# Performance work log

Measured on AMD Instinct MI355X. Metric: run time of the kernel, lower is better.

The kernel has to match this reference:

```python
import jax, jax.numpy as jnp
import numpy as np

N_SLOTS = 256   # memory slots
M_UNITS = 32    # memory word size
CTRL = 256      # LSTM controller units
N_IN = 8        # input features
N_OUT = 8
N_SHIFTS = 1
SHIFT_W = 2 * N_SHIFTS + 1          # 3 shift weights
ADDR = M_UNITS + 2 + SHIFT_W + 1    # key + beta + gate + shift + gamma = 38
CLIP = 20.0
EPS = 1e-8


def _lstm(x, h, c, Wk, Wr, b):
    z = x @ Wk + h @ Wr + b
    i, f, g, o = jnp.split(z, 4, axis=-1)  # keras gate order: i, f, c, o
    c = jax.nn.sigmoid(f) * c + jax.nn.sigmoid(i) * jnp.tanh(g)
    h = jax.nn.sigmoid(o) * jnp.tanh(c)
    return h, c


def _address(ho, w_prev, M):
    # ho: [B, ADDR] raw head outputs; M: [B, N, Mu]; w_prev: [B, N]
    k = jnp.tanh(ho[:, :M_UNITS])
    beta = jax.nn.softplus(ho[:, M_UNITS:M_UNITS + 1])
    g = jax.nn.sigmoid(ho[:, M_UNITS + 1:M_UNITS + 2])
    s = jax.nn.softmax(ho[:, M_UNITS + 2:M_UNITS + 2 + SHIFT_W], axis=-1)
    gamma = 1.0 + jax.nn.softplus(ho[:, ADDR - 1:ADDR])
    # content addressing via cosine similarity
    sim = jnp.einsum('bnm,bm->bn', M, k)
    sim = sim / (jnp.linalg.norm(M, axis=-1) * jnp.linalg.norm(k, axis=-1, keepdims=True) + EPS)
    w_c = jax.nn.softmax(beta * sim, axis=-1)
    # interpolation gate
    w_g = g * w_c + (1.0 - g) * w_prev
    # circular shift convolution over offsets [-N_SHIFTS..N_SHIFTS]
    w_s = sum(s[:, j:j + 1] * jnp.roll(w_g, j - N_SHIFTS, axis=-1) for j in range(SHIFT_W))
    # sharpening
    w_p = w_s ** gamma
    return w_p / (jnp.sum(w_p, axis=-1, keepdims=True) + EPS)


def setup_inputs() -> dict:
    key = jax.random.key(0)
    ks = jax.random.split(key, 10)
    B, T = 512, 64
    in_dim = N_IN + M_UNITS  # 40
    def w(k, shape, fan_in):
        return jax.random.normal(k, shape, jnp.float32) / np.sqrt(fan_in)
    return {
        'X': jax.random.normal(ks[0], (B, T, N_IN), jnp.float32),
        'lstm_Wk': w(ks[1], (in_dim, 4 * CTRL), in_dim),
        'lstm_Wr': w(ks[2], (CTRL, 4 * CTRL), CTRL),
        'lstm_b': jnp.zeros((4 * CTRL,), jnp.float32),
        'read_W': w(ks[3], (CTRL, ADDR), CTRL),
        'read_b': jnp.zeros((ADDR,), jnp.float32),
        'write_W': w(ks[4], (CTRL, ADDR + 2 * M_UNITS), CTRL),
        'write_b': jnp.zeros((ADDR + 2 * M_UNITS,), jnp.float32),
        'out_W': w(ks[5], (M_UNITS + CTRL, N_OUT), M_UNITS + CTRL),
        'out_b': jnp.zeros((N_OUT,), jnp.float32),
        'read_init': jax.random.normal(ks[6], (1, M_UNITS), jnp.float32),
        'wr_init': jax.random.normal(ks[7], (1, N_SLOTS), jnp.float32),
        'ww_init': jax.random.normal(ks[8], (1, N_SLOTS), jnp.float32),
    }


def reference(X, lstm_Wk, lstm_Wr, lstm_b, read_W, read_b, write_W, write_b,
              out_W, out_b, read_init, wr_init, ww_init):
    B = X.shape[0]
    M0 = jnp.full((B, N_SLOTS, M_UNITS), 1e-6, X.dtype)
    R0 = jnp.broadcast_to(jnp.tanh(read_init), (B, M_UNITS))
    Wr0 = jnp.broadcast_to(jax.nn.softmax(wr_init, axis=-1), (B, N_SLOTS))
    Ww0 = jnp.broadcast_to(jax.nn.softmax(ww_init, axis=-1), (B, N_SLOTS))
    h0 = jnp.zeros((B, CTRL), X.dtype)
    c0 = jnp.zeros((B, CTRL), X.dtype)

    def step(carry, x):
        M, R, Wr, Ww, h, c = carry
        h, c = _lstm(jnp.concatenate([x, R], axis=1), h, c, lstm_Wk, lstm_Wr, lstm_b)
        Z = jnp.clip(h, -CLIP, CLIP)
        # read head (uses pre-write memory, as in cell.call)
        Wr = _address(Z @ read_W + read_b, Wr, M)
        R = jnp.einsum('bn,bnm->bm', Wr, M)
        # write head: erase then add
        wo = Z @ write_W + write_b
        Ww = _address(wo[:, :ADDR], Ww, M)
        E = jax.nn.sigmoid(wo[:, ADDR:ADDR + M_UNITS])
        A = jnp.tanh(wo[:, ADDR + M_UNITS:ADDR + 2 * M_UNITS])
        M = M * (1.0 - jnp.einsum('bn,bm->bnm', Ww, E)) + jnp.einsum('bn,bm->bnm', Ww, A)
        Y = jnp.clip(jnp.concatenate([R, Z], axis=1) @ out_W + out_b, -CLIP, CLIP)
        return (M, R, Wr, Ww, h, c), Y

    _, Ys = jax.lax.scan(step, (M0, R0, Wr0, Ww0, h0, c0), jnp.swapaxes(X, 0, 1))
    return jnp.swapaxes(Ys, 0, 1)  # [B, T, N_OUT]
```

## Files before the change

### kernel.cpp

```cpp
#include <hip/hip_runtime.h>
#include <math.h>


#define NSLOT  256
#define MU     32
#define MPAD   33
#define TSTEPS 64
#define EPSF   1e-8f

__device__ __forceinline__ float sigf(float x){ return 1.0f/(1.0f + expf(-x)); }
__device__ __forceinline__ float softplusf_(float x){ return fmaxf(x,0.0f) + log1pf(expf(-fabsf(x))); }

__device__ __forceinline__ float wred_sum(float v){
  #pragma unroll
  for (int m = 32; m >= 1; m >>= 1) v += __shfl_xor(v, m, 64);
  return v;
}
__device__ __forceinline__ float wred_max(float v){
  #pragma unroll
  for (int m = 32; m >= 1; m >>= 1) v = fmaxf(v, __shfl_xor(v, m, 64));
  return v;
}

__device__ __forceinline__ float grp_red_sum(float v, float* red, int wave, int lane, int g2){
  v = wred_sum(v);
  if (lane == 0) red[wave] = v;
  __syncthreads();
  return red[4*g2] + red[4*g2+1] + red[4*g2+2] + red[4*g2+3];
}
__device__ __forceinline__ float grp_red_max(float v, float* red, int wave, int lane, int g2){
  v = wred_max(v);
  if (lane == 0) red[wave] = v;
  __syncthreads();
  return fmaxf(fmaxf(red[4*g2], red[4*g2+1]), fmaxf(red[4*g2+2], red[4*g2+3]));
}

struct Smem {
  float M[2][NSLOT][MPAD];
  float zp[2][2][1024];
  float h[2][256];
  float c[2][256];
  float hob[2][140];
  float xcat[2][40];
  float wr[2][NSLOT];
  float ww[2][NSLOT];
  float wg[2][2][NSLOT];
  float k[2][2][MU];
  float E[2][MU];
  float A[2][MU];
  float R[2][MU];
  float hpart[2][2][140];
  float rpart[2][8][MU];
  float red[3][8];
};

__device__ void address_head(int g2, int n2, int wave, int lane, int head,
                             const float* ho, float* wst, const float* Mg,
                             Smem& s)
{
  float beta  = softplusf_(ho[32]);
  float gg    = sigf(ho[33]);
  float r0 = ho[34], r1 = ho[35], r2 = ho[36];
  float m3 = fmaxf(r0, fmaxf(r1, r2));
  float e0 = expf(r0-m3), e1 = expf(r1-m3), e2 = expf(r2-m3);
  float inv3 = 1.0f/(e0+e1+e2);
  float s0 = e0*inv3, s1 = e1*inv3, s2 = e2*inv3;
  float gamma = 1.0f + softplusf_(ho[37]);

  float* kbuf  = &s.k[head][g2][0];
  float* wgbuf = &s.wg[head][g2][0];

  if (n2 < MU) kbuf[n2] = tanhf(ho[n2]);
  __syncthreads();

  float kn = 0.0f;
  #pragma unroll
  for (int m = 0; m < MU; ++m){ float kv = kbuf[m]; kn = fmaf(kv, kv, kn); }
  kn = sqrtf(kn);

  const float* Mr = Mg + n2*MPAD;
  float dot = 0.0f, mm = 0.0f;
  #pragma unroll
  for (int m = 0; m < MU; ++m){ float mv = Mr[m]; dot = fmaf(mv, kbuf[m], dot); mm = fmaf(mv, mv, mm); }
  float sim = dot / (sqrtf(mm)*kn + EPSF);

  float bs = beta * sim;
  float mx = grp_red_max(bs, s.red[0], wave, lane, g2);
  float ex = expf(bs - mx);
  float sm = grp_red_sum(ex, s.red[1], wave, lane, g2);
  float wc = ex / sm;

  float wgv = fmaf(gg, wc, (1.0f - gg)*wst[n2]);
  wgbuf[n2] = wgv;
  __syncthreads();

  float ws = s0*wgbuf[(n2+1)&255] + s1*wgbuf[n2] + s2*wgbuf[(n2-1)&255];

  float wp = powf(ws, gamma);
  float sp = grp_red_sum(wp, s.red[2], wave, lane, g2);
  wst[n2] = wp / (sp + EPSF);
}

__global__ __launch_bounds__(512)
void ntm_fused(const float* __restrict__ X,
               const float* __restrict__ Wk,   const float* __restrict__ Wr,
               const float* __restrict__ Lb,
               const float* __restrict__ rW,   const float* __restrict__ rb,
               const float* __restrict__ wW,   const float* __restrict__ wb,
               const float* __restrict__ oW,   const float* __restrict__ ob,
               const float* __restrict__ rInit,
               const float* __restrict__ wrI,  const float* __restrict__ wwI,
               float* __restrict__ Y)
{
  __shared__ Smem s;

  const int tid  = threadIdx.x;
  const int g2   = tid >> 8;
  const int n2   = tid & 255;
  const int wave = tid >> 6;
  const int lane = tid & 63;
  const int hf   = g2;
  const int bB   = blockIdx.x * 2;

  {
    for (int m = 0; m < MU; ++m) s.M[g2][n2][m] = 1e-6f;
    s.h[g2][n2] = 0.0f;
    s.c[g2][n2] = 0.0f;
    if (n2 < MU) s.R[g2][n2] = tanhf(rInit[n2]);
    float mx = -1e30f;
    for (int i = 0; i < NSLOT; ++i) mx = fmaxf(mx, wrI[i]);
    float sm = 0.0f;
    for (int i = 0; i < NSLOT; ++i) sm += expf(wrI[i] - mx);
    s.wr[g2][n2] = expf(wrI[n2] - mx) / sm;
    mx = -1e30f;
    for (int i = 0; i < NSLOT; ++i) mx = fmaxf(mx, wwI[i]);
    sm = 0.0f;
    for (int i = 0; i < NSLOT; ++i) sm += expf(wwI[i] - mx);
    s.ww[g2][n2] = expf(wwI[n2] - mx) / sm;
  }
  __syncthreads();

  for (int t = 0; t < TSTEPS; ++t) {
    if (n2 < 40) {
      s.xcat[g2][n2] = (n2 < 8) ? X[((bB + g2)*TSTEPS + t)*8 + n2]
                                : s.R[g2][n2 - 8];
    }
    __syncthreads();

    {
      const int c0 = n2 * 4;
      float a0x=0.f,a0y=0.f,a0z=0.f,a0w=0.f;
      float a1x=0.f,a1y=0.f,a1z=0.f,a1w=0.f;
      if (hf == 0) {
        #pragma unroll 4
        for (int i = 0; i < 40; ++i) {
          float4 w = *(const float4*)&Wk[i*1024 + c0];
          float x0 = s.xcat[0][i], x1 = s.xcat[1][i];
          a0x=fmaf(w.x,x0,a0x); a0y=fmaf(w.y,x0,a0y); a0z=fmaf(w.z,x0,a0z); a0w=fmaf(w.w,x0,a0w);
          a1x=fmaf(w.x,x1,a1x); a1y=fmaf(w.y,x1,a1y); a1z=fmaf(w.z,x1,a1z); a1w=fmaf(w.w,x1,a1w);
        }
        #pragma unroll 4
        for (int i = 0; i < 108; ++i) {
          float4 w = *(const float4*)&Wr[i*1024 + c0];
          float h0 = s.h[0][i], h1 = s.h[1][i];
          a0x=fmaf(w.x,h0,a0x); a0y=fmaf(w.y,h0,a0y); a0z=fmaf(w.z,h0,a0z); a0w=fmaf(w.w,h0,a0w);
          a1x=fmaf(w.x,h1,a1x); a1y=fmaf(w.y,h1,a1y); a1z=fmaf(w.z,h1,a1z); a1w=fmaf(w.w,h1,a1w);
        }
        float4 b = *(const float4*)&Lb[c0];
        a0x+=b.x; a0y+=b.y; a0z+=b.z; a0w+=b.w;
        a1x+=b.x; a1y+=b.y; a1z+=b.z; a1w+=b.w;
      } else {
        #pragma unroll 4
        for (int i = 108; i < 256; ++i) {
          float4 w = *(const float4*)&Wr[i*1024 + c0];
          float h0 = s.h[0][i], h1 = s.h[1][i];
          a0x=fmaf(w.x,h0,a0x); a0y=fmaf(w.y,h0,a0y); a0z=fmaf(w.z,h0,a0z); a0w=fmaf(w.w,h0,a0w);
          a1x=fmaf(w.x,h1,a1x); a1y=fmaf(w.y,h1,a1y); a1z=fmaf(w.z,h1,a1z); a1w=fmaf(w.w,h1,a1w);
        }
      }
      float* z0 = &s.zp[hf][0][c0];
      float* z1 = &s.zp[hf][1][c0];
      z0[0]=a0x; z0[1]=a0y; z0[2]=a0z; z0[3]=a0w;
      z1[0]=a1x; z1[1]=a1y; z1[2]=a1z; z1[3]=a1w;
    }
    __syncthreads();

    {
      float zi = s.zp[0][g2][n2      ] + s.zp[1][g2][n2      ];
      float zf = s.zp[0][g2][n2 + 256] + s.zp[1][g2][n2 + 256];
      float zg = s.zp[0][g2][n2 + 512] + s.zp[1][g2][n2 + 512];
      float zo = s.zp[0][g2][n2 + 768] + s.zp[1][g2][n2 + 768];
      float cn = sigf(zf)*s.c[g2][n2] + sigf(zi)*tanhf(zg);
      float hn = sigf(zo)*tanhf(cn);
      s.c[g2][n2] = cn;
      s.h[g2][n2] = hn;
    }
    __syncthreads();

    if (n2 < 140) {
      const float* Wp; int stride, cc;
      if (n2 < 38) { Wp = rW; stride = 38;  cc = n2; }
      else         { Wp = wW; stride = 102; cc = n2 - 38; }
      const int i0 = hf * 128;
      float acc0 = 0.0f, acc1 = 0.0f;
      #pragma unroll 4
      for (int ii = 0; ii < 128; ++ii) {
        int i = i0 + ii;
        float wv = Wp[i*stride + cc];
        acc0 = fmaf(wv, s.h[0][i], acc0);
        acc1 = fmaf(wv, s.h[1][i], acc1);
      }
      s.hpart[hf][0][n2] = acc0;
      s.hpart[hf][1][n2] = acc1;
    }
    __syncthreads();
    if (n2 < 140) {
      float bias = (n2 < 38) ? rb[n2] : wb[n2 - 38];
      s.hob[g2][n2] = s.hpart[0][g2][n2] + s.hpart[1][g2][n2] + bias;
    }
    __syncthreads();

    if (n2 < MU) {
      s.E[g2][n2] = sigf(s.hob[g2][76 + n2]);
      s.A[g2][n2] = tanhf(s.hob[g2][108 + n2]);
    }

    address_head(g2, n2, wave, lane, 0, &s.hob[g2][0],  &s.wr[g2][0],
                 &s.M[g2][0][0], s);
    address_head(g2, n2, wave, lane, 1, &s.hob[g2][38], &s.ww[g2][0],
                 &s.M[g2][0][0], s);

    {
      const int chunk = n2 >> 5;
      const int m     = n2 & 31;
      const float* Mg = &s.M[g2][0][0];
      const int nb = chunk * 32;
      float acc = 0.0f;
      #pragma unroll 4
      for (int nn = 0; nn < 32; ++nn) {
        int n = nb + nn;
        acc = fmaf(s.wr[g2][n], Mg[n*MPAD + m], acc);
      }
      s.rpart[g2][chunk][m] = acc;
    }
    __syncthreads();
    if (n2 < MU) {
      float r = 0.0f;
      #pragma unroll
      for (int c = 0; c < 8; ++c) r += s.rpart[g2][c][n2];
      s.R[g2][n2] = r;
    }
    __syncthreads();

    {
      float wwn = s.ww[g2][n2];
      float* Mr = &s.M[g2][n2][0];
      #pragma unroll
      for (int m = 0; m < MU; ++m) {
        Mr[m] = Mr[m] * (1.0f - wwn*s.E[g2][m]) + wwn*s.A[g2][m];
      }
    }

    {
      const int o = n2 >> 5;
      const int l = n2 & 31;
      float acc = 0.0f;
      #pragma unroll
      for (int ss = 0; ss < 9; ++ss) {
        int j = l + 32*ss;
        float v = (j < 32) ? s.R[g2][j] : s.h[g2][j - 32];
        acc = fmaf(v, oW[j*8 + o], acc);
      }
      #pragma unroll
      for (int m = 16; m >= 1; m >>= 1) acc += __shfl_xor(acc, m, 64);
      if (l == 0) {
        float y = acc + ob[o];
        y = fminf(fmaxf(y, -20.0f), 20.0f);
        Y[((bB + g2)*TSTEPS + t)*8 + o] = y;
      }
    }
    __syncthreads();
  }
}

extern "C" void kernel_launch(void* const* d_in, const int* in_sizes, int n_in,
                              void* d_out, int out_size, void* d_ws, size_t ws_size,
                              hipStream_t stream)
{
  const float* X     = (const float*)d_in[0];
  const float* Wk    = (const float*)d_in[1];
  const float* Wr    = (const float*)d_in[2];
  const float* Lb    = (const float*)d_in[3];
  const float* rW    = (const float*)d_in[4];
  const float* rb    = (const float*)d_in[5];
  const float* wW    = (const float*)d_in[6];
  const float* wb    = (const float*)d_in[7];
  const float* oW    = (const float*)d_in[8];
  const float* ob    = (const float*)d_in[9];
  const float* rInit = (const float*)d_in[10];
  const float* wrI   = (const float*)d_in[11];
  const float* wwI   = (const float*)d_in[12];
  float* Y = (float*)d_out;

  hipLaunchKernelGGL(ntm_fused, dim3(256), dim3(512), 0, stream,
                     X, Wk, Wr, Lb, rW, rb, wW, wb, oW, ob, rInit, wrI, wwI, Y);
}
```

Measured before the change: 1.860 ms.

## Double block to 1024 threads and split LSTM matvec four ways along K

The block grows from 512 to 1024 threads. The LSTM gate matvec is now split into four K-slices: 10 input rows plus 64 recurrent rows per quarter. The recurrent loop reads h as float4 and loads four weight rows per iteration. The bias add moves into the gate reduction, and the head projection, read and memory update stages spread their work over all threads. Addressing runs with duplicated thread groups writing identical values. The aim is more memory-level parallelism for the per-step weight streaming, at the cost of more LDS for partial sums and extra reduction work.

```diff
diff --git a/kernel.cpp b/kernel.cpp
--- a/kernel.cpp
+++ b/kernel.cpp
@@ -22,22 +22,9 @@
   return v;
 }
 
-__device__ __forceinline__ float grp_red_sum(float v, float* red, int wave, int lane, int g2){
-  v = wred_sum(v);
-  if (lane == 0) red[wave] = v;
-  __syncthreads();
-  return red[4*g2] + red[4*g2+1] + red[4*g2+2] + red[4*g2+3];
-}
-__device__ __forceinline__ float grp_red_max(float v, float* red, int wave, int lane, int g2){
-  v = wred_max(v);
-  if (lane == 0) red[wave] = v;
-  __syncthreads();
-  return fmaxf(fmaxf(red[4*g2], red[4*g2+1]), fmaxf(red[4*g2+2], red[4*g2+3]));
-}
-
-struct Smem {
+struct __align__(16) Smem {
   float M[2][NSLOT][MPAD];
-  float zp[2][2][1024];
+  float zp[4][2][1024];
   float h[2][256];
   float c[2][256];
   float hob[2][140];
@@ -49,12 +36,27 @@
   float E[2][MU];
   float A[2][MU];
   float R[2][MU];
-  float hpart[2][2][140];
-  float rpart[2][8][MU];
-  float red[3][8];
+  float hpart[4][2][140];
+  float rpart[2][16][32];
+  float red[3][16];
 };
 
-__device__ void address_head(int g2, int n2, int wave, int lane, int head,
+__device__ __forceinline__ float grp_red_sum(float v, float* red, int wave, int lane, int g2a){
+  v = wred_sum(v);
+  if (lane == 0) red[wave] = v;
+  __syncthreads();
+  const int b = g2a*8;
+  return red[b] + red[b+1] + red[b+2] + red[b+3];
+}
+__device__ __forceinline__ float grp_red_max(float v, float* red, int wave, int lane, int g2a){
+  v = wred_max(v);
+  if (lane == 0) red[wave] = v;
+  __syncthreads();
+  const int b = g2a*8;
+  return fmaxf(fmaxf(red[b], red[b+1]), fmaxf(red[b+2], red[b+3]));
+}
+
+__device__ void address_head(int g2a, int n2, int wave, int lane, int head,
                              const float* ho, float* wst, const float* Mg,
                              Smem& s)
 {
@@ -67,8 +69,8 @@
   float s0 = e0*inv3, s1 = e1*inv3, s2 = e2*inv3;
   float gamma = 1.0f + softplusf_(ho[37]);
 
-  float* kbuf  = &s.k[head][g2][0];
-  float* wgbuf = &s.wg[head][g2][0];
+  float* kbuf  = &s.k[head][g2a][0];
+  float* wgbuf = &s.wg[head][g2a][0];
 
   if (n2 < MU) kbuf[n2] = tanhf(ho[n2]);
   __syncthreads();
@@ -85,9 +87,9 @@
   float sim = dot / (sqrtf(mm)*kn + EPSF);
 
   float bs = beta * sim;
-  float mx = grp_red_max(bs, s.red[0], wave, lane, g2);
+  float mx = grp_red_max(bs, s.red[0], wave, lane, g2a);
   float ex = expf(bs - mx);
-  float sm = grp_red_sum(ex, s.red[1], wave, lane, g2);
+  float sm = grp_red_sum(ex, s.red[1], wave, lane, g2a);
   float wc = ex / sm;
 
   float wgv = fmaf(gg, wc, (1.0f - gg)*wst[n2]);
@@ -97,11 +99,11 @@
   float ws = s0*wgbuf[(n2+1)&255] + s1*wgbuf[n2] + s2*wgbuf[(n2-1)&255];
 
   float wp = powf(ws, gamma);
-  float sp = grp_red_sum(wp, s.red[2], wave, lane, g2);
+  float sp = grp_red_sum(wp, s.red[2], wave, lane, g2a);
   wst[n2] = wp / (sp + EPSF);
 }
 
-__global__ __launch_bounds__(512)
+__global__ __launch_bounds__(1024)
 void ntm_fused(const float* __restrict__ X,
                const float* __restrict__ Wk,   const float* __restrict__ Wr,
                const float* __restrict__ Lb,
@@ -115,35 +117,36 @@
   __shared__ Smem s;
 
   const int tid  = threadIdx.x;
-  const int g2   = tid >> 8;
+  const int q    = tid >> 8;
   const int n2   = tid & 255;
   const int wave = tid >> 6;
   const int lane = tid & 63;
-  const int hf   = g2;
+  const int gh   = q & 1;
+  const int g2a  = tid >> 9;
   const int bB   = blockIdx.x * 2;
 
-  {
-    for (int m = 0; m < MU; ++m) s.M[g2][n2][m] = 1e-6f;
-    s.h[g2][n2] = 0.0f;
-    s.c[g2][n2] = 0.0f;
-    if (n2 < MU) s.R[g2][n2] = tanhf(rInit[n2]);
+  if (tid < 512) {
+    for (int m = 0; m < MU; ++m) s.M[gh][n2][m] = 1e-6f;
+    s.h[gh][n2] = 0.0f;
+    s.c[gh][n2] = 0.0f;
+    if (n2 < MU) s.R[gh][n2] = tanhf(rInit[n2]);
     float mx = -1e30f;
     for (int i = 0; i < NSLOT; ++i) mx = fmaxf(mx, wrI[i]);
     float sm = 0.0f;
     for (int i = 0; i < NSLOT; ++i) sm += expf(wrI[i] - mx);
-    s.wr[g2][n2] = expf(wrI[n2] - mx) / sm;
+    s.wr[gh][n2] = expf(wrI[n2] - mx) / sm;
     mx = -1e30f;
     for (int i = 0; i < NSLOT; ++i) mx = fmaxf(mx, wwI[i]);
     sm = 0.0f;
     for (int i = 0; i < NSLOT; ++i) sm += expf(wwI[i] - mx);
-    s.ww[g2][n2] = expf(wwI[n2] - mx) / sm;
+    s.ww[gh][n2] = expf(wwI[n2] - mx) / sm;
   }
   __syncthreads();
 
   for (int t = 0; t < TSTEPS; ++t) {
-    if (n2 < 40) {
-      s.xcat[g2][n2] = (n2 < 8) ? X[((bB + g2)*TSTEPS + t)*8 + n2]
-                                : s.R[g2][n2 - 8];
+    if (tid < 512 && n2 < 40) {
+      s.xcat[gh][n2] = (n2 < 8) ? X[((bB + gh)*TSTEPS + t)*8 + n2]
+                                : s.R[gh][n2 - 8];
     }
     __syncthreads();
 
@@ -151,49 +154,48 @@
       const int c0 = n2 * 4;
       float a0x=0.f,a0y=0.f,a0z=0.f,a0w=0.f;
       float a1x=0.f,a1y=0.f,a1z=0.f,a1w=0.f;
-      if (hf == 0) {
-        #pragma unroll 4
-        for (int i = 0; i < 40; ++i) {
-          float4 w = *(const float4*)&Wk[i*1024 + c0];
-          float x0 = s.xcat[0][i], x1 = s.xcat[1][i];
-          a0x=fmaf(w.x,x0,a0x); a0y=fmaf(w.y,x0,a0y); a0z=fmaf(w.z,x0,a0z); a0w=fmaf(w.w,x0,a0w);
-          a1x=fmaf(w.x,x1,a1x); a1y=fmaf(w.y,x1,a1y); a1z=fmaf(w.z,x1,a1z); a1w=fmaf(w.w,x1,a1w);
-        }
-        #pragma unroll 4
-        for (int i = 0; i < 108; ++i) {
-          float4 w = *(const float4*)&Wr[i*1024 + c0];
-          float h0 = s.h[0][i], h1 = s.h[1][i];
-          a0x=fmaf(w.x,h0,a0x); a0y=fmaf(w.y,h0,a0y); a0z=fmaf(w.z,h0,a0z); a0w=fmaf(w.w,h0,a0w);
-          a1x=fmaf(w.x,h1,a1x); a1y=fmaf(w.y,h1,a1y); a1z=fmaf(w.z,h1,a1z); a1w=fmaf(w.w,h1,a1w);
-        }
-        float4 b = *(const float4*)&Lb[c0];
-        a0x+=b.x; a0y+=b.y; a0z+=b.z; a0w+=b.w;
-        a1x+=b.x; a1y+=b.y; a1z+=b.z; a1w+=b.w;
-      } else {
-        #pragma unroll 4
-        for (int i = 108; i < 256; ++i) {
-          float4 w = *(const float4*)&Wr[i*1024 + c0];
-          float h0 = s.h[0][i], h1 = s.h[1][i];
-          a0x=fmaf(w.x,h0,a0x); a0y=fmaf(w.y,h0,a0y); a0z=fmaf(w.z,h0,a0z); a0w=fmaf(w.w,h0,a0w);
-          a1x=fmaf(w.x,h1,a1x); a1y=fmaf(w.y,h1,a1y); a1z=fmaf(w.z,h1,a1z); a1w=fmaf(w.w,h1,a1w);
-        }
-      }
-      float* z0 = &s.zp[hf][0][c0];
-      float* z1 = &s.zp[hf][1][c0];
-      z0[0]=a0x; z0[1]=a0y; z0[2]=a0z; z0[3]=a0w;
-      z1[0]=a1x; z1[1]=a1y; z1[2]=a1z; z1[3]=a1w;
-    }
-    __syncthreads();
-
-    {
-      float zi = s.zp[0][g2][n2      ] + s.zp[1][g2][n2      ];
-      float zf = s.zp[0][g2][n2 + 256] + s.zp[1][g2][n2 + 256];
-      float zg = s.zp[0][g2][n2 + 512] + s.zp[1][g2][n2 + 512];
-      float zo = s.zp[0][g2][n2 + 768] + s.zp[1][g2][n2 + 768];
-      float cn = sigf(zf)*s.c[g2][n2] + sigf(zi)*tanhf(zg);
+      const int kb = 10*q;
+      #pragma unroll
+      for (int ii = 0; ii < 10; ++ii) {
+        const int i = kb + ii;
+        float4 w = *(const float4*)&Wk[i*1024 + c0];
+        float x0 = s.xcat[0][i], x1 = s.xcat[1][i];
+        a0x=fmaf(w.x,x0,a0x); a0y=fmaf(w.y,x0,a0y); a0z=fmaf(w.z,x0,a0z); a0w=fmaf(w.w,x0,a0w);
+        a1x=fmaf(w.x,x1,a1x); a1y=fmaf(w.y,x1,a1y); a1z=fmaf(w.z,x1,a1z); a1w=fmaf(w.w,x1,a1w);
+      }
+      const int rb4 = 16*q;
+      #pragma unroll 2
+      for (int i4 = 0; i4 < 16; ++i4) {
+        const int r = (rb4 + i4)*4;
+        float4 h0 = *(const float4*)&s.h[0][r];
+        float4 h1 = *(const float4*)&s.h[1][r];
+        float4 w0 = *(const float4*)&Wr[(r+0)*1024 + c0];
+        float4 w1 = *(const float4*)&Wr[(r+1)*1024 + c0];
+        float4 w2 = *(const float4*)&Wr[(r+2)*1024 + c0];
+        float4 w3 = *(const float4*)&Wr[(r+3)*1024 + c0];
+        a0x=fmaf(w0.x,h0.x,a0x); a0y=fmaf(w0.y,h0.x,a0y); a0z=fmaf(w0.z,h0.x,a0z); a0w=fmaf(w0.w,h0.x,a0w);
+        a1x=fmaf(w0.x,h1.x,a1x); a1y=fmaf(w0.y,h1.x,a1y); a1z=fmaf(w0.z,h1.x,a1z); a1w=fmaf(w0.w,h1.x,a1w);
+        a0x=fmaf(w1.x,h0.y,a0x); a0y=fmaf(w1.y,h0.y,a0y); a0z=fmaf(w1.z,h0.y,a0z); a0w=fmaf(w1.w,h0.y,a0w);
+        a1x=fmaf(w1.x,h1.y,a1x); a1y=fmaf(w1.y,h1.y,a1y); a1z=fmaf(w1.z,h1.y,a1z); a1w=fmaf(w1.w,h1.y,a1w);
+        a0x=fmaf(w2.x,h0.z,a0x); a0y=fmaf(w2.y,h0.z,a0y); a0z=fmaf(w2.z,h0.z,a0z); a0w=fmaf(w2.w,h0.z,a0w);
+        a1x=fmaf(w2.x,h1.z,a1x); a1y=fmaf(w2.y,h1.z,a1y); a1z=fmaf(w2.z,h1.z,a1z); a1w=fmaf(w2.w,h1.z,a1w);
+        a0x=fmaf(w3.x,h0.w,a0x); a0y=fmaf(w3.y,h0.w,a0y); a0z=fmaf(w3.z,h0.w,a0z); a0w=fmaf(w3.w,h0.w,a0w);
+        a1x=fmaf(w3.x,h1.w,a1x); a1y=fmaf(w3.y,h1.w,a1y); a1z=fmaf(w3.z,h1.w,a1z); a1w=fmaf(w3.w,h1.w,a1w);
+      }
+      *(float4*)&s.zp[q][0][c0] = make_float4(a0x,a0y,a0z,a0w);
+      *(float4*)&s.zp[q][1][c0] = make_float4(a1x,a1y,a1z,a1w);
+    }
+    __syncthreads();
+
+    if (tid < 512) {
+      float zi = s.zp[0][gh][n2      ]+s.zp[1][gh][n2      ]+s.zp[2][gh][n2      ]+s.zp[3][gh][n2      ] + Lb[n2      ];
+      float zf = s.zp[0][gh][n2 + 256]+s.zp[1][gh][n2 + 256]+s.zp[2][gh][n2 + 256]+s.zp[3][gh][n2 + 256] + Lb[n2 + 256];
+      float zg = s.zp[0][gh][n2 + 512]+s.zp[1][gh][n2 + 512]+s.zp[2][gh][n2 + 512]+s.zp[3][gh][n2 + 512] + Lb[n2 + 512];
+      float zo = s.zp[0][gh][n2 + 768]+s.zp[1][gh][n2 + 768]+s.zp[2][gh][n2 + 768]+s.zp[3][gh][n2 + 768] + Lb[n2 + 768];
+      float cn = sigf(zf)*s.c[gh][n2] + sigf(zi)*tanhf(zg);
       float hn = sigf(zo)*tanhf(cn);
-      s.c[g2][n2] = cn;
-      s.h[g2][n2] = hn;
+      s.c[gh][n2] = cn;
+      s.h[gh][n2] = hn;
     }
     __syncthreads();
 
@@ -201,74 +203,81 @@
       const float* Wp; int stride, cc;
       if (n2 < 38) { Wp = rW; stride = 38;  cc = n2; }
       else         { Wp = wW; stride = 102; cc = n2 - 38; }
-      const int i0 = hf * 128;
+      const int i0 = q * 64;
       float acc0 = 0.0f, acc1 = 0.0f;
       #pragma unroll 4
-      for (int ii = 0; ii < 128; ++ii) {
-        int i = i0 + ii;
+      for (int ii = 0; ii < 64; ++ii) {
+        const int i = i0 + ii;
         float wv = Wp[i*stride + cc];
         acc0 = fmaf(wv, s.h[0][i], acc0);
         acc1 = fmaf(wv, s.h[1][i], acc1);
       }
-      s.hpart[hf][0][n2] = acc0;
-      s.hpart[hf][1][n2] = acc1;
-    }
-    __syncthreads();
-    if (n2 < 140) {
+      s.hpart[q][0][n2] = acc0;
+      s.hpart[q][1][n2] = acc1;
+    }
+    __syncthreads();
+    if (tid < 512 && n2 < 140) {
       float bias = (n2 < 38) ? rb[n2] : wb[n2 - 38];
-      s.hob[g2][n2] = s.hpart[0][g2][n2] + s.hpart[1][g2][n2] + bias;
-    }
-    __syncthreads();
-
-    if (n2 < MU) {
-      s.E[g2][n2] = sigf(s.hob[g2][76 + n2]);
-      s.A[g2][n2] = tanhf(s.hob[g2][108 + n2]);
-    }
-
-    address_head(g2, n2, wave, lane, 0, &s.hob[g2][0],  &s.wr[g2][0],
-                 &s.M[g2][0][0], s);
-    address_head(g2, n2, wave, lane, 1, &s.hob[g2][38], &s.ww[g2][0],
-                 &s.M[g2][0][0], s);
+      s.hob[gh][n2] = s.hpart[0][gh][n2] + s.hpart[1][gh][n2]
+                    + s.hpart[2][gh][n2] + s.hpart[3][gh][n2] + bias;
+    }
+    __syncthreads();
+
+    if (tid < 512 && n2 < MU) {
+      s.E[gh][n2] = sigf(s.hob[gh][76 + n2]);
+      s.A[gh][n2] = tanhf(s.hob[gh][108 + n2]);
+    }
+
+    address_head(g2a, n2, wave, lane, 0, &s.hob[g2a][0],  &s.wr[g2a][0],
+                 &s.M[g2a][0][0], s);
+    address_head(g2a, n2, wave, lane, 1, &s.hob[g2a][38], &s.ww[g2a][0],
+                 &s.M[g2a][0][0], s);
 
     {
-      const int chunk = n2 >> 5;
-      const int m     = n2 & 31;
-      const float* Mg = &s.M[g2][0][0];
-      const int nb = chunk * 32;
+      const int gg  = tid >> 9;
+      const int c16 = (tid >> 5) & 15;
+      const int m   = tid & 31;
+      const float* Mg = &s.M[gg][0][0];
+      const int nb = c16 * 16;
       float acc = 0.0f;
       #pragma unroll 4
-      for (int nn = 0; nn < 32; ++nn) {
-        int n = nb + nn;
-        acc = fmaf(s.wr[g2][n], Mg[n*MPAD + m], acc);
-      }
-      s.rpart[g2][chunk][m] = acc;
-    }
-    __syncthreads();
-    if (n2 < MU) {
+      for (int nn = 0; nn < 16; ++nn) {
+        const int n = nb + nn;
+        acc = fmaf(s.wr[gg][n], Mg[n*MPAD + m], acc);
+      }
+      s.rpart[gg][c16][m] = acc;
+    }
+    __syncthreads();
+    if (tid < 512 && n2 < MU) {
       float r = 0.0f;
       #pragma unroll
-      for (int c = 0; c < 8; ++c) r += s.rpart[g2][c][n2];
-      s.R[g2][n2] = r;
+      for (int c = 0; c < 16; ++c) r += s.rpart[gh][c][n2];
+      s.R[gh][n2] = r;
     }
     __syncthreads();
 
     {
-      float wwn = s.ww[g2][n2];
-      float* Mr = &s.M[g2][n2][0];
-      #pragma unroll
-      for (int m = 0; m < MU; ++m) {
-        Mr[m] = Mr[m] * (1.0f - wwn*s.E[g2][m]) + wwn*s.A[g2][m];
-      }
-    }
-
-    {
+      const int gg   = tid >> 9;
+      const int row  = tid & 255;
+      const int half = (tid >> 8) & 1;
+      const float wwn = s.ww[gg][row];
+      float* Mr       = &s.M[gg][row][half*16];
+      const float* Eg = &s.E[gg][half*16];
+      const float* Ag = &s.A[gg][half*16];
+      #pragma unroll
+      for (int m = 0; m < 16; ++m) {
+        Mr[m] = Mr[m] * (1.0f - wwn*Eg[m]) + wwn*Ag[m];
+      }
+    }
+
+    if (tid < 512) {
       const int o = n2 >> 5;
       const int l = n2 & 31;
       float acc = 0.0f;
       #pragma unroll
       for (int ss = 0; ss < 9; ++ss) {
-        int j = l + 32*ss;
-        float v = (j < 32) ? s.R[g2][j] : s.h[g2][j - 32];
+        const int j = l + 32*ss;
+        float v = (j < 32) ? s.R[gh][j] : s.h[gh][j - 32];
         acc = fmaf(v, oW[j*8 + o], acc);
       }
       #pragma unroll
@@ -276,7 +285,7 @@
       if (l == 0) {
         float y = acc + ob[o];
         y = fminf(fmaxf(y, -20.0f), 20.0f);
-        Y[((bB + g2)*TSTEPS + t)*8 + o] = y;
+        Y[((bB + gh)*TSTEPS + t)*8 + o] = y;
       }
     }
     __syncthreads();
@@ -302,6 +311,6 @@
   const float* wwI   = (const float*)d_in[12];
   float* Y = (float*)d_out;
 
-  hipLaunchKernelGGL(ntm_fused, dim3(256), dim3(512), 0, stream,
+  hipLaunchKernelGGL(ntm_fused, dim3(256), dim3(1024), 0, stream,
                      X, Wk, Wr, Lb, rW, rb, wW, wb, oW, ob, rInit, wrI, wwI, Y);
 }
```

Measured after the change: 3.962 ms. +113.1%, slower.
